# Optimization experiments

Measured on AMD Instinct MI355X. Metric: run time of the kernel, lower is better.

## Reference

```python
import jax, jax.numpy as jnp
import numpy as np

N = 10000
E = 320000


def spmm(edge_row, edge_col, edge_val, support):
    # out[r] = sum_{edges (r,c)} val * support[c]  -- torch.spmm(adj, support)
    gathered = support[edge_col] * edge_val[:, None]  # [E, d]
    return jax.ops.segment_sum(gathered, edge_row, num_segments=N)


def setup_inputs() -> dict:
    key = jax.random.key(0)
    ks = jax.random.split(key, 10)
    nfeat, nhid, classes = 512, 512, 256
    return {
        "x": jax.random.normal(ks[0], (N, nfeat), dtype=jnp.float32),
        "edge_row": jax.random.randint(ks[1], (E,), 0, N, dtype=jnp.int32),
        "edge_col": jax.random.randint(ks[2], (E,), 0, N, dtype=jnp.int32),
        "edge_val": jax.random.uniform(ks[3], (E,), dtype=jnp.float32),
        "W0": jax.random.normal(ks[4], (nfeat, nhid), dtype=jnp.float32) / np.sqrt(nfeat),
        "W1": jax.random.normal(ks[5], (2 * nhid, nhid), dtype=jnp.float32) / np.sqrt(2 * nhid),
        "W2": jax.random.normal(ks[6], (2 * nhid, classes), dtype=jnp.float32) / np.sqrt(2 * nhid),
        "b0": jax.random.normal(ks[7], (nhid,), dtype=jnp.float32) * 0.02,
        "b1": jax.random.normal(ks[8], (nhid,), dtype=jnp.float32) * 0.02,
        "b2": jax.random.normal(ks[9], (classes,), dtype=jnp.float32) * 0.02,
    }


def reference(x, edge_row, edge_col, edge_val, W0, W1, W2, b0, b1, b2):
    # layer 0: Linear(nfeat, nhid, bias=False) -> spmm -> +bias
    x_ = spmm(edge_row, edge_col, edge_val, x @ W0) + b0
    h = jax.nn.relu(x_)
    x = jnp.concatenate([h, x_], axis=-1)  # skip=True concat
    # layer 1: Linear(2*nhid, nhid, bias=False) -> spmm -> +bias
    x_ = spmm(edge_row, edge_col, edge_val, x @ W1) + b1
    h = jax.nn.relu(x_)
    x = jnp.concatenate([h, x_], axis=-1)
    # final layer: Linear(2*nhid, classes, bias=False) -> spmm -> +bias
    out = spmm(edge_row, edge_col, edge_val, x @ W2) + b2
    return out
```

## Files before the change

kernel.cpp:

```cpp
#include <hip/hip_runtime.h>
#include <hip/hip_bf16.h>
#include <stdint.h>
#include <type_traits>


typedef _Float16 half8 __attribute__((ext_vector_type(8)));
typedef _Float16 half4 __attribute__((ext_vector_type(4)));
typedef float    f32x4 __attribute__((ext_vector_type(4)));

#define N_NODES 10000
#define M_PAD   10112
#define N_EDGES 320000

__device__ __forceinline__ void async16(const void* g, void* l) {
    __builtin_amdgcn_global_load_lds(
        (const __attribute__((address_space(1))) void*)g,
        (__attribute__((address_space(3))) void*)l, 16, 0, 0);
}

template <int TM, int TN>
__device__ __forceinline__ void gemm_body(
    int bx, int by,
    const _Float16* __restrict__ A,
    const _Float16* __restrict__ Bt,
    _Float16* __restrict__ C,
    int K, int Nc)
{
    constexpr int WM = TM / 2;
    constexpr int WN = TN / 2;
    constexpr int MT = WM / 16;
    constexpr int NT = WN / 16;
    constexpr int NCHUNK = (TM + TN) / 16;
    constexpr int CA = TM / 16;

    __shared__ _Float16 As[2][TM * 32];
    __shared__ _Float16 Bs[2][TN * 32];

    const int t    = threadIdx.x;
    const int lane = t & 63;
    const int wid  = t >> 6;
    const int wrow = wid >> 1;
    const int wcol = wid & 1;
    const int quad = lane >> 4;
    const int l15  = lane & 15;

    const int rowBase = by * TM;
    const int colBase = bx * TN;

    const int rIn = lane >> 2;
    const int cIn = (lane & 3) * 8;

    f32x4 acc[MT][NT];
#pragma unroll
    for (int m = 0; m < MT; ++m)
#pragma unroll
        for (int n = 0; n < NT; ++n)
            acc[m][n] = (f32x4){0.f, 0.f, 0.f, 0.f};

    auto stage = [&](int buf, int k0) {
#pragma unroll
        for (int p = 0; p < NCHUNK / 4; ++p) {
            const int c = wid + p * 4;
            if (c < CA) {
                const int r = c * 16 + rIn;
                async16(&A[(size_t)(rowBase + r) * K + k0 + cIn], &As[buf][c * 512]);
            } else {
                const int r = (c - CA) * 16 + rIn;
                async16(&Bt[(size_t)(colBase + r) * K + k0 + cIn], &Bs[buf][(c - CA) * 512]);
            }
        }
    };

    const int nk = K >> 5;
    stage(0, 0);

    for (int i = 0; i < nk; ++i) {
        __syncthreads();
        if (i + 1 < nk) stage((i + 1) & 1, (i + 1) << 5);

        const int b = i & 1;
        half8 af[MT], bf[NT];
#pragma unroll
        for (int m = 0; m < MT; ++m)
            af[m] = *(const half8*)(&As[b][(wrow * WM + m * 16 + l15) * 32 + quad * 8]);
#pragma unroll
        for (int n = 0; n < NT; ++n)
            bf[n] = *(const half8*)(&Bs[b][(wcol * WN + n * 16 + l15) * 32 + quad * 8]);

#pragma unroll
        for (int m = 0; m < MT; ++m)
#pragma unroll
            for (int n = 0; n < NT; ++n)
                acc[m][n] = __builtin_amdgcn_mfma_f32_16x16x32_f16(
                    af[m], bf[n], acc[m][n], 0, 0, 0);
    }

#pragma unroll
    for (int m = 0; m < MT; ++m) {
#pragma unroll
        for (int n = 0; n < NT; ++n) {
            int col = colBase + wcol * WN + n * 16 + l15;
#pragma unroll
            for (int r = 0; r < 4; ++r) {
                int row = rowBase + wrow * WM + m * 16 + quad * 4 + r;
                C[(size_t)row * Nc + col] = (_Float16)acc[m][n][r];
            }
        }
    }
}

template <int TM, int TN>
__device__ __forceinline__ void gemm_body8(
    int bx, int by,
    const _Float16* __restrict__ A,
    const _Float16* __restrict__ Bt,
    _Float16* __restrict__ C,
    int K, int Nc)
{
    constexpr int WM = TM / 2;
    constexpr int WN = TN / 4;
    constexpr int MT = WM / 16;
    constexpr int NT = WN / 16;
    constexpr int NCHUNK = (TM + TN) / 16;
    constexpr int CA = TM / 16;

    __shared__ _Float16 As[2][TM * 32];
    __shared__ _Float16 Bs[2][TN * 32];

    const int t    = threadIdx.x;
    const int lane = t & 63;
    const int wid  = t >> 6;
    const int wrow = wid >> 2;
    const int wcol = wid & 3;
    const int quad = lane >> 4;
    const int l15  = lane & 15;

    const int rowBase = by * TM;
    const int colBase = bx * TN;

    const int rIn = lane >> 2;
    const int cIn = (lane & 3) * 8;

    f32x4 acc[MT][NT];
#pragma unroll
    for (int m = 0; m < MT; ++m)
#pragma unroll
        for (int n = 0; n < NT; ++n)
            acc[m][n] = (f32x4){0.f, 0.f, 0.f, 0.f};

    auto stage = [&](int buf, int k0) {
#pragma unroll
        for (int p = 0; p < NCHUNK / 8; ++p) {
            const int c = wid + p * 8;
            if (c < CA) {
                const int r = c * 16 + rIn;
                async16(&A[(size_t)(rowBase + r) * K + k0 + cIn], &As[buf][c * 512]);
            } else {
                const int r = (c - CA) * 16 + rIn;
                async16(&Bt[(size_t)(colBase + r) * K + k0 + cIn], &Bs[buf][(c - CA) * 512]);
            }
        }
    };

    const int nk = K >> 5;
    stage(0, 0);

    for (int i = 0; i < nk; ++i) {
        __syncthreads();
        if (i + 1 < nk) stage((i + 1) & 1, (i + 1) << 5);

        const int b = i & 1;
        half8 af[MT], bf[NT];
#pragma unroll
        for (int m = 0; m < MT; ++m)
            af[m] = *(const half8*)(&As[b][(wrow * WM + m * 16 + l15) * 32 + quad * 8]);
#pragma unroll
        for (int n = 0; n < NT; ++n)
            bf[n] = *(const half8*)(&Bs[b][(wcol * WN + n * 16 + l15) * 32 + quad * 8]);

#pragma unroll
        for (int m = 0; m < MT; ++m)
#pragma unroll
            for (int n = 0; n < NT; ++n)
                acc[m][n] = __builtin_amdgcn_mfma_f32_16x16x32_f16(
                    af[m], bf[n], acc[m][n], 0, 0, 0);
    }

#pragma unroll
    for (int m = 0; m < MT; ++m) {
#pragma unroll
        for (int n = 0; n < NT; ++n) {
            int col = colBase + wcol * WN + n * 16 + l15;
#pragma unroll
            for (int r = 0; r < 4; ++r) {
                int row = rowBase + wrow * WM + m * 16 + quad * 4 + r;
                C[(size_t)row * Nc + col] = (_Float16)acc[m][n][r];
            }
        }
    }
}

template <int TM, int TN>
__global__ __launch_bounds__(256) void gemm_f16_t(
    const _Float16* __restrict__ A,
    const _Float16* __restrict__ Bt,
    _Float16* __restrict__ C,
    int K, int Nc)
{
    gemm_body<TM, TN>(blockIdx.x, blockIdx.y, A, Bt, C, K, Nc);
}

template <int TM, int TN>
__global__ __launch_bounds__(512) void gemm_f16_t8(
    const _Float16* __restrict__ A,
    const _Float16* __restrict__ Bt,
    _Float16* __restrict__ C,
    int K, int Nc)
{
    gemm_body8<TM, TN>(blockIdx.x, blockIdx.y, A, Bt, C, K, Nc);
}

#define PREP_XB   5000
#define PREP_W0B  256
#define PREP_W1B  512
#define PREP_W2B  256
#define HIST_B    1250
#define PREPH_BLKS (PREP_XB + PREP_W0B + PREP_W1B + PREP_W2B + HIST_B)

__device__ __forceinline__ void tile_tr(const float* __restrict__ W,
                                        _Float16* __restrict__ Wt,
                                        int K, int Nc, int tR, int tC, int t) {
    __shared__ float tile[32][33];
    const int ty = t >> 5, tx = t & 31;
#pragma unroll
    for (int it = 0; it < 4; ++it)
        tile[ty + 8 * it][tx] = W[(size_t)(tR * 32 + ty + 8 * it) * Nc + tC * 32 + tx];
    __syncthreads();
#pragma unroll
    for (int it = 0; it < 4; ++it)
        Wt[(size_t)(tC * 32 + ty + 8 * it) * K + tR * 32 + tx] =
            (_Float16)tile[tx][ty + 8 * it];
}

__global__ __launch_bounds__(256) void prep_hist(
    const float* __restrict__ x,  _Float16* __restrict__ Xh,
    const float* __restrict__ W0, _Float16* __restrict__ W0t,
    const float* __restrict__ W1, _Float16* __restrict__ W1t,
    const float* __restrict__ W2, _Float16* __restrict__ W2t,
    const int* __restrict__ edge_row, int* __restrict__ counts) {
    const int t = threadIdx.x;
    int b = blockIdx.x;
    if (b < PREP_XB) {
        int i = b * 256 + t;
        f32x4 v = *(const f32x4*)(x + (size_t)i * 4);
        half4 h;
        h[0] = (_Float16)v[0]; h[1] = (_Float16)v[1];
        h[2] = (_Float16)v[2]; h[3] = (_Float16)v[3];
        *(half4*)(Xh + (size_t)i * 4) = h;
        return;
    }
    b -= PREP_XB;
    if (b < PREP_W0B) { tile_tr(W0, W0t, 512, 512, b >> 4, b & 15, t); return; }
    b -= PREP_W0B;
    if (b < PREP_W1B) { tile_tr(W1, W1t, 1024, 512, b >> 4, b & 15, t); return; }
    b -= PREP_W1B;
    if (b < PREP_W2B) { tile_tr(W2, W2t, 1024, 256, b >> 3, b & 7, t); return; }
    b -= PREP_W2B;
    {
        int i = b * 256 + t;
        if (i < N_EDGES) atomicAdd(&counts[edge_row[i]], 1);
    }
}

__global__ __launch_bounds__(1024) void scan_rowptr(
    const int* __restrict__ counts,
    int* __restrict__ row_ptr,
    int* __restrict__ cursor) {
    const int t = threadIdx.x, lane = t & 63, wid = t >> 6;
    const int base = t * 10;
    int c[10];
    int s = 0;
    if (base < N_NODES) {
#pragma unroll
        for (int j = 0; j < 10; ++j) { s += counts[base + j]; c[j] = s; }
    }
    int v = s;
#pragma unroll
    for (int d = 1; d < 64; d <<= 1) {
        int u = __shfl_up(v, d, 64);
        if (lane >= d) v += u;
    }
    __shared__ int wsum[16];
    if (lane == 63) wsum[wid] = v;
    __syncthreads();
    if (t == 0) {
        int run = 0;
#pragma unroll
        for (int i = 0; i < 16; ++i) { int x = wsum[i]; wsum[i] = run; run += x; }
    }
    __syncthreads();
    if (base < N_NODES) {
        const int excl = wsum[wid] + v - s;
        row_ptr[base] = excl; cursor[base] = excl;
#pragma unroll
        for (int j = 1; j < 10; ++j) {
            int val = excl + c[j - 1];
            row_ptr[base + j] = val; cursor[base + j] = val;
        }
    }
    if (t == 0) row_ptr[N_NODES] = N_EDGES;
}

#define G0_BLKS 316
#define SCAT_BLKS 625

__global__ __launch_bounds__(512) void gemm0_scatter(
    const _Float16* __restrict__ Xh,
    const _Float16* __restrict__ W0t,
    _Float16* __restrict__ S,
    const int* __restrict__ rows,
    const int* __restrict__ cols,
    const float* __restrict__ vals,
    int* __restrict__ cursor,
    float2* __restrict__ ev) {
    int b = blockIdx.x;
    if (b < G0_BLKS) {
        gemm_body8<128, 128>(b & 3, b >> 2, Xh, W0t, S, 512, 512);
        return;
    }
    b -= G0_BLKS;
    int i = b * 512 + threadIdx.x;
    if (i < N_EDGES) {
        int r = rows[i];
        int p = atomicAdd(&cursor[r], 1);
        ev[p] = make_float2(__int_as_float(cols[i]), vals[i]);
    }
}

template <int D, bool FINAL>
__global__ __launch_bounds__(256) void spmm_slice(
    const int* __restrict__ row_ptr,
    const float2* __restrict__ ev,
    const _Float16* __restrict__ S,
    const float* __restrict__ bias,
    _Float16* __restrict__ Hout,
    float* __restrict__ Fout)
{
    constexpr int NS = D / 128;
    const int s  = blockIdx.x & (NS - 1);
    const int rq = blockIdx.x / NS;
    const int w  = threadIdx.x >> 6;
    const int row = rq * 4 + w;
    const int lane = threadIdx.x & 63;
    const int g = lane >> 4;
    const int l = lane & 15;

    const int r0 = row_ptr[row];
    const int r1 = row_ptr[row + 1];

    float acc[8];
#pragma unroll
    for (int j = 0; j < 8; ++j) acc[j] = 0.f;

    const _Float16* __restrict__ Sb = S + s * 128 + l * 8;

    int e = r0 + g;
    for (; e + 12 < r1; e += 16) {
        float2 p[4];
        half8  v[4];
#pragma unroll
        for (int u = 0; u < 4; ++u) p[u] = ev[e + 4 * u];
#pragma unroll
        for (int u = 0; u < 4; ++u)
            v[u] = *(const half8*)(Sb + (size_t)__float_as_int(p[u].x) * D);
#pragma unroll
        for (int u = 0; u < 4; ++u)
#pragma unroll
            for (int j = 0; j < 8; ++j) acc[j] += p[u].y * (float)v[u][j];
    }
    for (; e + 4 < r1; e += 8) {
        float2 p0 = ev[e];
        float2 p1 = ev[e + 4];
        half8 v0 = *(const half8*)(Sb + (size_t)__float_as_int(p0.x) * D);
        half8 v1 = *(const half8*)(Sb + (size_t)__float_as_int(p1.x) * D);
#pragma unroll
        for (int j = 0; j < 8; ++j) {
            acc[j] += p0.y * (float)v0[j];
            acc[j] += p1.y * (float)v1[j];
        }
    }
    if (e < r1) {
        float2 p0 = ev[e];
        half8 v0 = *(const half8*)(Sb + (size_t)__float_as_int(p0.x) * D);
#pragma unroll
        for (int j = 0; j < 8; ++j) acc[j] += p0.y * (float)v0[j];
    }

#pragma unroll
    for (int j = 0; j < 8; ++j) {
        acc[j] += __shfl_xor(acc[j], 16, 64);
        acc[j] += __shfl_xor(acc[j], 32, 64);
    }

    const int f0 = s * 128 + l * 8;
    f32x4 b0 = *(const f32x4*)(bias + f0);
    f32x4 b1 = *(const f32x4*)(bias + f0 + 4);

    if constexpr (FINAL) {
        if (g == 0) {
            f32x4 o = {acc[0] + b0[0], acc[1] + b0[1], acc[2] + b0[2], acc[3] + b0[3]};
            *(f32x4*)(Fout + (size_t)row * D + f0) = o;
        } else if (g == 1) {
            f32x4 o = {acc[4] + b1[0], acc[5] + b1[1], acc[6] + b1[2], acc[7] + b1[3]};
            *(f32x4*)(Fout + (size_t)row * D + f0 + 4) = o;
        }
    } else {
        float v[8];
#pragma unroll
        for (int j = 0; j < 4; ++j) v[j] = acc[j] + b0[j];
#pragma unroll
        for (int j = 0; j < 4; ++j) v[4 + j] = acc[4 + j] + b1[j];
        if (g == 0) {
            half8 h;
#pragma unroll
            for (int j = 0; j < 8; ++j) h[j] = (_Float16)(v[j] > 0.f ? v[j] : 0.f);
            *(half8*)(Hout + (size_t)row * (2 * D) + f0) = h;
        } else if (g == 1) {
            half8 h;
#pragma unroll
            for (int j = 0; j < 8; ++j) h[j] = (_Float16)v[j];
            *(half8*)(Hout + (size_t)row * (2 * D) + D + f0) = h;
        }
    }
}

static inline char* alignp(char* p, size_t a) {
    return (char*)(((uintptr_t)p + a - 1) & ~(uintptr_t)(a - 1));
}

extern "C" void kernel_launch(void* const* d_in, const int* in_sizes, int n_in,
                              void* d_out, int out_size, void* d_ws, size_t ws_size,
                              hipStream_t stream) {
    const float* x        = (const float*)d_in[0];
    const int*   edge_row = (const int*)d_in[1];
    const int*   edge_col = (const int*)d_in[2];
    const float* edge_val = (const float*)d_in[3];
    const float* W0 = (const float*)d_in[4];
    const float* W1 = (const float*)d_in[5];
    const float* W2 = (const float*)d_in[6];
    const float* b0 = (const float*)d_in[7];
    const float* b1 = (const float*)d_in[8];
    const float* b2 = (const float*)d_in[9];
    float* out = (float*)d_out;

    const int E = N_EDGES;

    char* p = (char*)d_ws;
    _Float16* Xh  = (_Float16*)alignp(p, 256);  p = (char*)(Xh  + (size_t)M_PAD * 512);
    _Float16* S   = (_Float16*)alignp(p, 256);  p = (char*)(S   + (size_t)M_PAD * 512);
    _Float16* H   = (_Float16*)alignp(p, 256);  p = (char*)(H   + (size_t)M_PAD * 1024);
    _Float16* W0t = (_Float16*)alignp(p, 256);  p = (char*)(W0t + (size_t)512 * 512);
    _Float16* W1t = (_Float16*)alignp(p, 256);  p = (char*)(W1t + (size_t)512 * 1024);
    _Float16* W2t = (_Float16*)alignp(p, 256);  p = (char*)(W2t + (size_t)256 * 1024);
    int*    counts  = (int*)alignp(p, 256);     p = (char*)(counts  + N_NODES);
    int*    row_ptr = (int*)alignp(p, 256);     p = (char*)(row_ptr + N_NODES + 1);
    int*    cursor  = (int*)alignp(p, 256);     p = (char*)(cursor  + N_NODES);
    float2* ev      = (float2*)alignp(p, 256);  p = (char*)(ev      + E);

    (void)hipMemsetAsync(counts, 0, N_NODES * sizeof(int), stream);
    prep_hist<<<PREPH_BLKS, 256, 0, stream>>>(x, Xh, W0, W0t, W1, W1t, W2, W2t,
                                              edge_row, counts);
    scan_rowptr<<<1, 1024, 0, stream>>>(counts, row_ptr, cursor);

    gemm0_scatter<<<G0_BLKS + SCAT_BLKS, 512, 0, stream>>>(
        Xh, W0t, S, edge_row, edge_col, edge_val, cursor, ev);
    spmm_slice<512, false><<<(N_NODES / 4) * 4, 256, 0, stream>>>(row_ptr, ev, S, b0, H, nullptr);
    gemm_f16_t8<128, 128><<<dim3(4, M_PAD / 128), 512, 0, stream>>>(H, W1t, S, 1024, 512);
    spmm_slice<512, false><<<(N_NODES / 4) * 4, 256, 0, stream>>>(row_ptr, ev, S, b1, H, nullptr);
    gemm_f16_t<64, 64><<<dim3(4, M_PAD / 64), 256, 0, stream>>>(H, W2t, S, 1024, 256);
    spmm_slice<256, true><<<(N_NODES / 4) * 2, 256, 0, stream>>>(row_ptr, ev, S, b2, nullptr, out);
}
```

Before: 268.8 us.

## Store pre-activation only and apply ReLU inside dual-weight GEMM

```diff
diff --git a/kernel.cpp b/kernel.cpp
--- a/kernel.cpp
+++ b/kernel.cpp
@@ -110,28 +110,30 @@
 }
 
 template <int TM, int TN>
-__device__ __forceinline__ void gemm_body8(
+__device__ __forceinline__ void gemm_dual(
     int bx, int by,
-    const _Float16* __restrict__ A,
+    const _Float16* __restrict__ Z,
     const _Float16* __restrict__ Bt,
     _Float16* __restrict__ C,
-    int K, int Nc)
+    int Nc)
 {
     constexpr int WM = TM / 2;
-    constexpr int WN = TN / 4;
+    constexpr int WN = TN / 2;
     constexpr int MT = WM / 16;
     constexpr int NT = WN / 16;
-    constexpr int NCHUNK = (TM + TN) / 16;
     constexpr int CA = TM / 16;
-
-    __shared__ _Float16 As[2][TM * 32];
-    __shared__ _Float16 Bs[2][TN * 32];
+    constexpr int CB = TN / 16;
+    constexpr int NCH = CA + 2 * CB;
+
+    __shared__ _Float16 As [2][TM * 32];
+    __shared__ _Float16 Bs0[2][TN * 32];
+    __shared__ _Float16 Bs1[2][TN * 32];
 
     const int t    = threadIdx.x;
     const int lane = t & 63;
     const int wid  = t >> 6;
-    const int wrow = wid >> 2;
-    const int wcol = wid & 3;
+    const int wrow = wid >> 1;
+    const int wcol = wid & 1;
     const int quad = lane >> 4;
     const int l15  = lane & 15;
 
@@ -150,40 +152,53 @@
 
     auto stage = [&](int buf, int k0) {
 #pragma unroll
-        for (int p = 0; p < NCHUNK / 8; ++p) {
-            const int c = wid + p * 8;
+        for (int p = 0; p < NCH / 4; ++p) {
+            const int c = wid + p * 4;
             if (c < CA) {
                 const int r = c * 16 + rIn;
-                async16(&A[(size_t)(rowBase + r) * K + k0 + cIn], &As[buf][c * 512]);
+                async16(&Z[(size_t)(rowBase + r) * 512 + k0 + cIn], &As[buf][c * 512]);
+            } else if (c < CA + CB) {
+                const int cc = c - CA;
+                const int r = cc * 16 + rIn;
+                async16(&Bt[(size_t)(colBase + r) * 1024 + k0 + cIn], &Bs0[buf][cc * 512]);
             } else {
-                const int r = (c - CA) * 16 + rIn;
-                async16(&Bt[(size_t)(colBase + r) * K + k0 + cIn], &Bs[buf][(c - CA) * 512]);
+                const int cc = c - CA - CB;
+                const int r = cc * 16 + rIn;
+                async16(&Bt[(size_t)(colBase + r) * 1024 + 512 + k0 + cIn], &Bs1[buf][cc * 512]);
             }
         }
     };
 
-    const int nk = K >> 5;
     stage(0, 0);
 
-    for (int i = 0; i < nk; ++i) {
+    for (int i = 0; i < 16; ++i) {
         __syncthreads();
-        if (i + 1 < nk) stage((i + 1) & 1, (i + 1) << 5);
+        if (i + 1 < 16) stage((i + 1) & 1, (i + 1) << 5);
 
         const int b = i & 1;
-        half8 af[MT], bf[NT];
+        half8 af[MT], ar[MT], bf0[NT], bf1[NT];
+#pragma unroll
+        for (int m = 0; m < MT; ++m) {
+            af[m] = *(const half8*)(&As[b][(wrow * WM + m * 16 + l15) * 32 + quad * 8]);
+#pragma unroll
+            for (int j = 0; j < 8; ++j)
+                ar[m][j] = af[m][j] > (_Float16)0 ? af[m][j] : (_Float16)0;
+        }
+#pragma unroll
+        for (int n = 0; n < NT; ++n) {
+            bf0[n] = *(const half8*)(&Bs0[b][(wcol * WN + n * 16 + l15) * 32 + quad * 8]);
+            bf1[n] = *(const half8*)(&Bs1[b][(wcol * WN + n * 16 + l15) * 32 + quad * 8]);
+        }
+
 #pragma unroll
         for (int m = 0; m < MT; ++m)
-            af[m] = *(const half8*)(&As[b][(wrow * WM + m * 16 + l15) * 32 + quad * 8]);
-#pragma unroll
-        for (int n = 0; n < NT; ++n)
-            bf[n] = *(const half8*)(&Bs[b][(wcol * WN + n * 16 + l15) * 32 + quad * 8]);
-
-#pragma unroll
-        for (int m = 0; m < MT; ++m)
-#pragma unroll
-            for (int n = 0; n < NT; ++n)
+#pragma unroll
+            for (int n = 0; n < NT; ++n) {
                 acc[m][n] = __builtin_amdgcn_mfma_f32_16x16x32_f16(
-                    af[m], bf[n], acc[m][n], 0, 0, 0);
+                    ar[m], bf0[n], acc[m][n], 0, 0, 0);
+                acc[m][n] = __builtin_amdgcn_mfma_f32_16x16x32_f16(
+                    af[m], bf1[n], acc[m][n], 0, 0, 0);
+            }
     }
 
 #pragma unroll
@@ -201,23 +216,13 @@
 }
 
 template <int TM, int TN>
-__global__ __launch_bounds__(256) void gemm_f16_t(
-    const _Float16* __restrict__ A,
+__global__ __launch_bounds__(256) void gemm_dual_k(
+    const _Float16* __restrict__ Z,
     const _Float16* __restrict__ Bt,
     _Float16* __restrict__ C,
-    int K, int Nc)
+    int Nc)
 {
-    gemm_body<TM, TN>(blockIdx.x, blockIdx.y, A, Bt, C, K, Nc);
-}
-
-template <int TM, int TN>
-__global__ __launch_bounds__(512) void gemm_f16_t8(
-    const _Float16* __restrict__ A,
-    const _Float16* __restrict__ Bt,
-    _Float16* __restrict__ C,
-    int K, int Nc)
-{
-    gemm_body8<TM, TN>(blockIdx.x, blockIdx.y, A, Bt, C, K, Nc);
+    gemm_dual<TM, TN>(blockIdx.x, blockIdx.y, Z, Bt, C, Nc);
 }
 
 #define PREP_XB   5000
@@ -311,10 +316,10 @@
     if (t == 0) row_ptr[N_NODES] = N_EDGES;
 }
 
-#define G0_BLKS 316
-#define SCAT_BLKS 625
-
-__global__ __launch_bounds__(512) void gemm0_scatter(
+#define G0_BLKS 632
+#define SCAT_BLKS 1250
+
+__global__ __launch_bounds__(256) void gemm0_scatter(
     const _Float16* __restrict__ Xh,
     const _Float16* __restrict__ W0t,
     _Float16* __restrict__ S,
@@ -325,11 +330,11 @@
     float2* __restrict__ ev) {
     int b = blockIdx.x;
     if (b < G0_BLKS) {
-        gemm_body8<128, 128>(b & 3, b >> 2, Xh, W0t, S, 512, 512);
+        gemm_body<64, 128>(b & 3, b >> 2, Xh, W0t, S, 512, 512);
         return;
     }
     b -= G0_BLKS;
-    int i = b * 512 + threadIdx.x;
+    int i = b * 256 + threadIdx.x;
     if (i < N_EDGES) {
         int r = rows[i];
         int p = atomicAdd(&cursor[r], 1);
@@ -343,7 +348,7 @@
     const float2* __restrict__ ev,
     const _Float16* __restrict__ S,
     const float* __restrict__ bias,
-    _Float16* __restrict__ Hout,
+    _Float16* __restrict__ Zout,
     float* __restrict__ Fout)
 {
     constexpr int NS = D / 128;
@@ -415,21 +420,13 @@
             *(f32x4*)(Fout + (size_t)row * D + f0 + 4) = o;
         }
     } else {
-        float v[8];
-#pragma unroll
-        for (int j = 0; j < 4; ++j) v[j] = acc[j] + b0[j];
-#pragma unroll
-        for (int j = 0; j < 4; ++j) v[4 + j] = acc[4 + j] + b1[j];
         if (g == 0) {
             half8 h;
 #pragma unroll
-            for (int j = 0; j < 8; ++j) h[j] = (_Float16)(v[j] > 0.f ? v[j] : 0.f);
-            *(half8*)(Hout + (size_t)row * (2 * D) + f0) = h;
-        } else if (g == 1) {
-            half8 h;
-#pragma unroll
-            for (int j = 0; j < 8; ++j) h[j] = (_Float16)v[j];
-            *(half8*)(Hout + (size_t)row * (2 * D) + D + f0) = h;
+            for (int j = 0; j < 4; ++j) h[j] = (_Float16)(acc[j] + b0[j]);
+#pragma unroll
+            for (int j = 0; j < 4; ++j) h[4 + j] = (_Float16)(acc[4 + j] + b1[j]);
+            *(half8*)(Zout + (size_t)row * D + f0) = h;
         }
     }
 }
@@ -458,7 +455,7 @@
     char* p = (char*)d_ws;
     _Float16* Xh  = (_Float16*)alignp(p, 256);  p = (char*)(Xh  + (size_t)M_PAD * 512);
     _Float16* S   = (_Float16*)alignp(p, 256);  p = (char*)(S   + (size_t)M_PAD * 512);
-    _Float16* H   = (_Float16*)alignp(p, 256);  p = (char*)(H   + (size_t)M_PAD * 1024);
+    _Float16* Z   = (_Float16*)alignp(p, 256);  p = (char*)(Z   + (size_t)M_PAD * 512);
     _Float16* W0t = (_Float16*)alignp(p, 256);  p = (char*)(W0t + (size_t)512 * 512);
     _Float16* W1t = (_Float16*)alignp(p, 256);  p = (char*)(W1t + (size_t)512 * 1024);
     _Float16* W2t = (_Float16*)alignp(p, 256);  p = (char*)(W2t + (size_t)256 * 1024);
@@ -472,11 +469,11 @@
                                               edge_row, counts);
     scan_rowptr<<<1, 1024, 0, stream>>>(counts, row_ptr, cursor);
 
-    gemm0_scatter<<<G0_BLKS + SCAT_BLKS, 512, 0, stream>>>(
+    gemm0_scatter<<<G0_BLKS + SCAT_BLKS, 256, 0, stream>>>(
         Xh, W0t, S, edge_row, edge_col, edge_val, cursor, ev);
-    spmm_slice<512, false><<<(N_NODES / 4) * 4, 256, 0, stream>>>(row_ptr, ev, S, b0, H, nullptr);
-    gemm_f16_t8<128, 128><<<dim3(4, M_PAD / 128), 512, 0, stream>>>(H, W1t, S, 1024, 512);
-    spmm_slice<512, false><<<(N_NODES / 4) * 4, 256, 0, stream>>>(row_ptr, ev, S, b1, H, nullptr);
-    gemm_f16_t<64, 64><<<dim3(4, M_PAD / 64), 256, 0, stream>>>(H, W2t, S, 1024, 256);
+    spmm_slice<512, false><<<(N_NODES / 4) * 4, 256, 0, stream>>>(row_ptr, ev, S, b0, Z, nullptr);
+    gemm_dual_k<64, 128><<<dim3(4, M_PAD / 64), 256, 0, stream>>>(Z, W1t, S, 512);
+    spmm_slice<512, false><<<(N_NODES / 4) * 4, 256, 0, stream>>>(row_ptr, ev, S, b1, Z, nullptr);
+    gemm_dual_k<64, 64><<<dim3(4, M_PAD / 64), 256, 0, stream>>>(Z, W2t, S, 256);
     spmm_slice<256, true><<<(N_NODES / 4) * 2, 256, 0, stream>>>(row_ptr, ev, S, b2, nullptr, out);
 }
```

After: 252.8 us. 1.06x faster.
